# Optimization experiments

Hardware: AMD Instinct MI355X
Metric: run time of the kernel (lower is better)

Reference implementation:

```python
import jax, jax.numpy as jnp
import numpy as np

B, S, D, H = 2, 2048, 512, 8
HD = D // H  # head_size = 64
EPS = 1e-5


def _layer_norm(x, g, b):
    m = jnp.mean(x, axis=-1, keepdims=True)
    v = jnp.mean(jnp.square(x - m), axis=-1, keepdims=True)
    return (x - m) * jax.lax.rsqrt(v + EPS) * g + b


def setup_inputs() -> dict:
    key = jax.random.key(0)
    ks = jax.random.split(key, 16)
    s_in = 1.0 / np.sqrt(D)
    s_ff = 1.0 / np.sqrt(4 * D)
    return {
        "x": jax.random.normal(ks[0], (B, S, D), jnp.float32),
        # per-head q/k/v projections stacked over heads: [H, D, HD]
        "Wq": jax.random.normal(ks[1], (H, D, HD), jnp.float32) * s_in,
        "bq": jax.random.normal(ks[2], (H, HD), jnp.float32) * s_in,
        "Wk": jax.random.normal(ks[3], (H, D, HD), jnp.float32) * s_in,
        "bk": jax.random.normal(ks[4], (H, HD), jnp.float32) * s_in,
        "Wv": jax.random.normal(ks[5], (H, D, HD), jnp.float32) * s_in,
        "bv": jax.random.normal(ks[6], (H, HD), jnp.float32) * s_in,
        "Wp": jax.random.normal(ks[7], (D, D), jnp.float32) * s_in,
        "bp": jax.random.normal(ks[8], (D,), jnp.float32) * s_in,
        "W1": jax.random.normal(ks[9], (D, 4 * D), jnp.float32) * s_in,
        "b1": jax.random.normal(ks[10], (4 * D,), jnp.float32) * s_in,
        "W2": jax.random.normal(ks[11], (4 * D, D), jnp.float32) * s_ff,
        "b2": jax.random.normal(ks[12], (D,), jnp.float32) * s_ff,
        "g1": jnp.ones((D,), jnp.float32),
        "be1": jnp.zeros((D,), jnp.float32),
        "g2": jnp.ones((D,), jnp.float32),
        "be2": jnp.zeros((D,), jnp.float32),
    }


def reference(x, Wq, bq, Wk, bk, Wv, bv, Wp, bp, W1, b1, W2, b2, g1, be1, g2, be2):
    # --- attention sublayer (pre-norm) ---
    xn = _layer_norm(x, g1, be1)                               # [B,S,D]
    q = jnp.einsum('bsd,hde->bhse', xn, Wq) + bq[None, :, None, :]
    k = jnp.einsum('bsd,hde->bhse', xn, Wk) + bk[None, :, None, :]
    v = jnp.einsum('bsd,hde->bhse', xn, Wv) + bv[None, :, None, :]
    # NOTE: original has NO 1/sqrt(head_size) scaling and NO mask
    scores = jnp.einsum('bhse,bhte->bhst', q, k)               # [B,H,S,S]
    w = jax.nn.softmax(scores, axis=-1)
    o = jnp.einsum('bhst,bhte->bhse', w, v)                    # [B,H,S,HD]
    o = o.transpose(0, 2, 1, 3).reshape(x.shape[0], x.shape[1], D)  # concat heads
    attn_out = o @ Wp + bp
    x = x + attn_out
    # --- MLP sublayer (pre-norm) ---
    xn2 = _layer_norm(x, g2, be2)
    h = jax.nn.relu(xn2 @ W1 + b1)
    x = x + (h @ W2 + b2)
    return x
```

## Files before the change

### kernel.cpp

```cpp
#include <hip/hip_runtime.h>
#include <hip/hip_bf16.h>

typedef unsigned short u16;
typedef unsigned long long u64t;
typedef __attribute__((ext_vector_type(8))) short bhalf8;
typedef __attribute__((ext_vector_type(4))) short bhalf4;
typedef __attribute__((ext_vector_type(4))) float f32x4;

#define MFMA16(a, b, c) __builtin_amdgcn_mfma_f32_16x16x32_bf16((a), (b), (c), 0, 0, 0)

#if __has_builtin(__builtin_amdgcn_mfma_f32_16x16x16bf16_1k)
#define HAVE_K16 1
#define MFMAK16(a, b, c) __builtin_amdgcn_mfma_f32_16x16x16bf16_1k((a), (b), (c), 0, 0, 0)
#elif __has_builtin(__builtin_amdgcn_mfma_f32_16x16x16_bf16)
#define HAVE_K16 1
#define MFMAK16(a, b, c) __builtin_amdgcn_mfma_f32_16x16x16_bf16((a), (b), (c), 0, 0, 0)
#else
#define HAVE_K16 0
#endif

#define BB 2
#define SS 2048
#define DD 512
#define HH 8
#define HD 64
#define NT (BB * SS)
#define LOG2E 1.44269504f

#if __has_builtin(__builtin_amdgcn_exp2f)
#define EXP2(x) __builtin_amdgcn_exp2f(x)
#else
#define EXP2(x) exp2f(x)
#endif

__device__ __forceinline__ u16 f2b(float f) {
    unsigned u = __builtin_bit_cast(unsigned, f);
    unsigned r = (u + 0x7fffu + ((u >> 16) & 1u)) >> 16;
    return (u16)r;
}

__device__ __forceinline__ void gl2lds16(const u16* g, u16* l) {
    u16* gn = (u16*)g;
    __builtin_amdgcn_global_load_lds((__attribute__((address_space(1))) void*)gn,
                                     (__attribute__((address_space(3))) void*)l, 16, 0, 0);
}

__global__ __launch_bounds__(256) void k_prep(const float* __restrict__ Wq, const float* __restrict__ Wk,
                                              const float* __restrict__ Wv, const float* __restrict__ Wp,
                                              const float* __restrict__ W1, const float* __restrict__ W2,
                                              const float* __restrict__ bq, const float* __restrict__ bk,
                                              const float* __restrict__ bv,
                                              u16* __restrict__ WqkvT, u16* __restrict__ WpT,
                                              u16* __restrict__ W1T, u16* __restrict__ W2T,
                                              float* __restrict__ biasqkv,
                                              const float* __restrict__ x, const float* __restrict__ g1,
                                              const float* __restrict__ be1, u16* __restrict__ xn) {
    int j = blockIdx.x;
    int t = threadIdx.x;
    if (j >= 3078) {
        int wave = t >> 6, lane = t & 63;
        int row = (j - 3078) * 4 + wave;
        const float* xr = x + (size_t)row * DD;
        int c = lane * 8;
        float4 v0 = *(const float4*)(xr + c);
        float4 v1 = *(const float4*)(xr + c + 4);
        float s  = v0.x + v0.y + v0.z + v0.w + v1.x + v1.y + v1.z + v1.w;
        float sq = v0.x*v0.x + v0.y*v0.y + v0.z*v0.z + v0.w*v0.w
                 + v1.x*v1.x + v1.y*v1.y + v1.z*v1.z + v1.w*v1.w;
#pragma unroll
        for (int m = 1; m < 64; m <<= 1) {
            s  += __shfl_xor(s, m);
            sq += __shfl_xor(sq, m);
        }
        float mean = s * (1.0f / DD);
        float var  = sq * (1.0f / DD) - mean * mean;
        float rstd = rsqrtf(var + 1e-5f);
        float4 g0 = *(const float4*)(g1 + c);
        float4 g4 = *(const float4*)(g1 + c + 4);
        float4 b0 = *(const float4*)(be1 + c);
        float4 b4 = *(const float4*)(be1 + c + 4);
        float xv[8] = {v0.x, v0.y, v0.z, v0.w, v1.x, v1.y, v1.z, v1.w};
        float gv[8] = {g0.x, g0.y, g0.z, g0.w, g4.x, g4.y, g4.z, g4.w};
        float bv2[8] = {b0.x, b0.y, b0.z, b0.w, b4.x, b4.y, b4.z, b4.w};
        union { bhalf8 v; u16 u[8]; } pk;
#pragma unroll
        for (int i = 0; i < 8; i++) pk.u[i] = f2b((xv[i] - mean) * rstd * gv[i] + bv2[i]);
        *(bhalf8*)(xn + (size_t)row * DD + c) = pk.v;
        return;
    }
    int tx = t & 31, ty = t >> 5;
    if (j >= 3072) {
        int i = (j - 3072) * 256 + ty * 32 + tx;
        biasqkv[i] = (i < 512) ? bq[i] : (i < 1024) ? bk[i - 512] : bv[i - 1024];
        return;
    }
    __shared__ float tile[32][33];
    const float* src; u16* dst; int R, C, tr, tc;
    if (j < 768) {
        int m = j >> 8, rem = j & 255, h = rem >> 5, tl = rem & 31;
        tr = tl >> 1; tc = tl & 1;
        src = (m == 0 ? Wq : (m == 1 ? Wk : Wv)) + h * 32768;
        dst = WqkvT + m * 262144 + h * 32768;
        R = 512; C = 64;
    } else if (j < 1024) { int tl = j - 768;  tr = tl >> 4; tc = tl & 15; src = Wp; dst = WpT; R = 512;  C = 512;  }
    else if (j < 2048)   { int tl = j - 1024; tr = tl >> 6; tc = tl & 63; src = W1; dst = W1T; R = 512;  C = 2048; }
    else                 { int tl = j - 2048; tr = tl >> 4; tc = tl & 15; src = W2; dst = W2T; R = 2048; C = 512;  }
    int c = tc * 32 + tx;
#pragma unroll
    for (int i = 0; i < 4; i++)
        tile[ty + i * 8][tx] = src[(size_t)(tr * 32 + ty + i * 8) * C + c];
    __syncthreads();
    int r2 = tr * 32 + tx;
#pragma unroll
    for (int i = 0; i < 4; i++)
        dst[(size_t)(tc * 32 + ty + i * 8) * R + r2] = f2b(tile[tx][ty + i * 8]);
}

__global__ __launch_bounds__(256) void k_layernorm(const float* __restrict__ x,
                                                   const float* __restrict__ g,
                                                   const float* __restrict__ be,
                                                   u16* __restrict__ out) {
    int wave = threadIdx.x >> 6, lane = threadIdx.x & 63;
    int row = blockIdx.x * 4 + wave;
    const float* xr = x + (size_t)row * DD;
    int c = lane * 8;
    float4 v0 = *(const float4*)(xr + c);
    float4 v1 = *(const float4*)(xr + c + 4);
    float s  = v0.x + v0.y + v0.z + v0.w + v1.x + v1.y + v1.z + v1.w;
    float sq = v0.x*v0.x + v0.y*v0.y + v0.z*v0.z + v0.w*v0.w
             + v1.x*v1.x + v1.y*v1.y + v1.z*v1.z + v1.w*v1.w;
#pragma unroll
    for (int m = 1; m < 64; m <<= 1) {
        s  += __shfl_xor(s, m);
        sq += __shfl_xor(sq, m);
    }
    float mean = s * (1.0f / DD);
    float var  = sq * (1.0f / DD) - mean * mean;
    float rstd = rsqrtf(var + 1e-5f);
    float4 g0 = *(const float4*)(g + c);
    float4 g1 = *(const float4*)(g + c + 4);
    float4 b0 = *(const float4*)(be + c);
    float4 b1 = *(const float4*)(be + c + 4);
    float xv[8] = {v0.x, v0.y, v0.z, v0.w, v1.x, v1.y, v1.z, v1.w};
    float gv[8] = {g0.x, g0.y, g0.z, g0.w, g1.x, g1.y, g1.z, g1.w};
    float bv[8] = {b0.x, b0.y, b0.z, b0.w, b1.x, b1.y, b1.z, b1.w};
    union { bhalf8 v; u16 u[8]; } pk;
#pragma unroll
    for (int i = 0; i < 8; i++) pk.u[i] = f2b((xv[i] - mean) * rstd * gv[i] + bv[i]);
    *(bhalf8*)(out + (size_t)row * DD + c) = pk.v;
}

template<int BM, int BN, int WR, int WC, int MI, int NI, int MODE>
__global__ __launch_bounds__(256) void k_gemm(const u16* __restrict__ A, const u16* __restrict__ Bt,
                                              const float* __restrict__ bias,
                                              int lda, int ldb, int kLen, int N,
                                              const float* __restrict__ resid,
                                              float* __restrict__ outF, u16* __restrict__ outB,
                                              u16* __restrict__ qd, u16* __restrict__ kd,
                                              u16* __restrict__ vtd) {
    constexpr int WM = MI * 16;
    constexpr int WN = NI * 16;
    static_assert(WR * WM == BM && WC * WN == BN && WR * WC == 4, "cfg");
    constexpr int ACH = BM / 32;
    constexpr int BCH = BN / 32;
    __shared__ u16 As[BM * 64];
    __shared__ u16 Bs[BN * 64];
    int t = threadIdx.x;
    int wave = t >> 6, lane = t & 63, quad = lane >> 4, l16 = lane & 15;
    int wr, wc;
    if (WC == 1)      { wr = wave; wc = 0; }
    else if (WR == 1) { wr = 0;    wc = wave; }
    else              { wr = wave >> 1; wc = wave & 1; }
    int m0 = blockIdx.y * BM, n0 = blockIdx.x * BN;

    f32x4 acc[MI][NI] = {};

    int srow = lane >> 3;
    int scol = (lane & 7) * 8;
    const u16* Ag = A  + (size_t)(m0 + srow) * lda + scol;
    const u16* Bg = Bt + (size_t)(n0 + srow) * ldb + scol;

    for (int k0 = 0; k0 < kLen; k0 += 64) {
        __syncthreads();
#pragma unroll
        for (int c = 0; c < ACH; c++) {
            int ch = wave * ACH + c;
            gl2lds16(Ag + (size_t)(ch * 8) * lda + k0, &As[ch * 512]);
        }
#pragma unroll
        for (int c = 0; c < BCH; c++) {
            int ch = wave * BCH + c;
            gl2lds16(Bg + (size_t)(ch * 8) * ldb + k0, &Bs[ch * 512]);
        }
        __syncthreads();
#pragma unroll
        for (int h = 0; h < 2; h++) {
            bhalf8 af[MI], bf[NI];
#pragma unroll
            for (int mi = 0; mi < MI; mi++)
                af[mi] = *(bhalf8*)&As[(wr * WM + mi * 16 + l16) * 64 + h * 32 + quad * 8];
#pragma unroll
            for (int ni = 0; ni < NI; ni++)
                bf[ni] = *(bhalf8*)&Bs[(wc * WN + ni * 16 + l16) * 64 + h * 32 + quad * 8];
#pragma unroll
            for (int mi = 0; mi < MI; mi++)
#pragma unroll
                for (int ni = 0; ni < NI; ni++)
                    acc[mi][ni] = MFMA16(af[mi], bf[ni], acc[mi][ni]);
        }
    }

#pragma unroll
    for (int mi = 0; mi < MI; mi++)
#pragma unroll
        for (int ni = 0; ni < NI; ni++) {
            f32x4 a = acc[mi][ni];
            int gc = n0 + wc * WN + ni * 16 + l16;
            int gr0 = m0 + wr * WM + mi * 16 + quad * 4;
            float bsv = bias[gc];
            if (MODE == 0) {
                int mm = gc >> 9, cc = gc & 511;
                int hh = cc >> 6, e = cc & 63;
                int b = gr0 >> 11, s0 = gr0 & 2047;
                if (mm == 2) {
                    u64t pk = 0;
#pragma unroll
                    for (int r = 0; r < 4; r++) pk |= (u64t)f2b(a[r] + bsv) << (16 * r);
                    *(u64t*)&vtd[((size_t)(b * HH + hh) * HD + e) * SS + s0] = pk;
                } else if (mm == 0) {
#pragma unroll
                    for (int r = 0; r < 4; r++)
                        qd[((size_t)(b * HH + hh) * SS + s0 + r) * HD + e] = f2b((a[r] + bsv) * LOG2E);
                } else {
#pragma unroll
                    for (int r = 0; r < 4; r++)
                        kd[((size_t)(b * HH + hh) * SS + s0 + r) * HD + e] = f2b(a[r] + bsv);
                }
            } else if (MODE == 1) {
#pragma unroll
                for (int r = 0; r < 4; r++) {
                    size_t idx = (size_t)(gr0 + r) * N + gc;
                    outF[idx] = a[r] + bsv + resid[idx];
                }
            } else {
#pragma unroll
                for (int r = 0; r < 4; r++)
                    outB[(size_t)(gr0 + r) * N + gc] = f2b(fmaxf(a[r] + bsv, 0.0f));
            }
        }
}

__global__ __launch_bounds__(512) void k_attention(const u16* __restrict__ q,
                                                   const u16* __restrict__ k,
                                                   const u16* __restrict__ vt,
                                                   float* __restrict__ Opart,
                                                   float* __restrict__ lsum) {
    __shared__ u16 sm[17920];
    u16* Ks = sm;
    u16* Vs = sm + 9216;
    float* Ored = (float*)sm;
    float* Lred = (float*)sm + 8192;

    int bh = blockIdx.x, qt = blockIdx.y, kspl = blockIdx.z;
    int t = threadIdx.x, wave = t >> 6, lane = t & 63, quad = lane >> 4, l16 = lane & 15;
    int g = wave >> 2, qw = wave & 3;
    const u16* qb = q  + (size_t)bh * SS * HD;
    const u16* kb = k  + (size_t)bh * SS * HD;
    const u16* vb = vt + (size_t)bh * HD * SS;

    bhalf8 qfa0, qfa1, qfb0, qfb1;
    {
        int r0 = qt * 128 + qw * 32 + l16;
        qfa0 = *(const bhalf8*)(qb + (size_t)r0 * HD + quad * 8);
        qfa1 = *(const bhalf8*)(qb + (size_t)r0 * HD + 32 + quad * 8);
        qfb0 = *(const bhalf8*)(qb + (size_t)(r0 + 16) * HD + quad * 8);
        qfb1 = *(const bhalf8*)(qb + (size_t)(r0 + 16) * HD + 32 + quad * 8);
    }

    f32x4 oacc[2][4] = {};
    float rsa = 0.f, rsb = 0.f;

    int kr = t >> 2, kc = (t & 3) * 16;
    int vr = t >> 3, vc = (t & 7) * 16;
    const u16* kp = kb + ((size_t)kspl * 1024 + kr) * HD + kc;
    const u16* vp = vb + (size_t)vr * SS + kspl * 1024 + vc;
    u16* ksd = &Ks[kr * 72 + kc];
    u16* vsd = &Vs[vr * 136 + vc];

    bhalf8 kreg[2], vreg[2];
#pragma unroll
    for (int i = 0; i < 2; i++) {
        kreg[i] = *(const bhalf8*)(kp + i * 8);
        vreg[i] = *(const bhalf8*)(vp + i * 8);
    }

    for (int it = 0; it < 8; it++) {
        __syncthreads();
#pragma unroll
        for (int i = 0; i < 2; i++) {
            *(bhalf8*)(ksd + i * 8) = kreg[i];
            *(bhalf8*)(vsd + i * 8) = vreg[i];
        }
        __syncthreads();
        if (it < 7) {
            const u16* kn = kp + (size_t)(it + 1) * 128 * HD;
            const u16* vn = vp + (it + 1) * 128;
#pragma unroll
            for (int i = 0; i < 2; i++) {
                kreg[i] = *(const bhalf8*)(kn + i * 8);
                vreg[i] = *(const bhalf8*)(vn + i * 8);
            }
        }

#pragma unroll
        for (int nt2 = 0; nt2 < 4; nt2++) {
            int nt = g * 4 + nt2;
            bhalf8 kf0 = *(bhalf8*)&Ks[(nt * 16 + l16) * 72 + quad * 8];
            bhalf8 kf1 = *(bhalf8*)&Ks[(nt * 16 + l16) * 72 + 32 + quad * 8];
            f32x4 sa = {}, sb = {};
            sa = MFMA16(kf0, qfa0, sa);
            sa = MFMA16(kf1, qfa1, sa);
            sb = MFMA16(kf0, qfb0, sb);
            sb = MFMA16(kf1, qfb1, sb);
#if HAVE_K16
            union { bhalf4 v; u16 u[4]; } pa, pb;
#pragma unroll
            for (int r = 0; r < 4; r++) {
                float p0 = EXP2(sa[r]);
                float p1 = EXP2(sb[r]);
                rsa += p0; rsb += p1;
                pa.u[r] = f2b(p0); pb.u[r] = f2b(p1);
            }
#pragma unroll
            for (int et = 0; et < 4; et++) {
                bhalf4 vf = *(bhalf4*)&Vs[(et * 16 + l16) * 136 + nt * 16 + quad * 4];
                oacc[0][et] = MFMAK16(pa.v, vf, oacc[0][et]);
                oacc[1][et] = MFMAK16(pb.v, vf, oacc[1][et]);
            }
#else
            union { bhalf8 v; u16 u[8]; } pa, pb;
#pragma unroll
            for (int r = 0; r < 4; r++) {
                float p0 = EXP2(sa[r]);
                float p1 = EXP2(sb[r]);
                rsa += p0; rsb += p1;
                pa.u[r] = f2b(p0); pb.u[r] = f2b(p1);
            }
#pragma unroll
            for (int r = 4; r < 8; r++) { pa.u[r] = 0; pb.u[r] = 0; }
#pragma unroll
            for (int et = 0; et < 4; et++) {
                union { bhalf8 v; bhalf4 h[2]; } vf;
                vf.h[0] = *(bhalf4*)&Vs[(et * 16 + l16) * 136 + nt * 16 + quad * 4];
                vf.h[1] = (bhalf4){0, 0, 0, 0};
                oacc[0][et] = MFMA16(pa.v, vf.v, oacc[0][et]);
                oacc[1][et] = MFMA16(pb.v, vf.v, oacc[1][et]);
            }
#endif
        }
    }

    rsa += __shfl_xor(rsa, 16); rsa += __shfl_xor(rsa, 32);
    rsb += __shfl_xor(rsb, 16); rsb += __shfl_xor(rsb, 32);

    __syncthreads();
    if (g == 1) {
#pragma unroll
        for (int qc = 0; qc < 2; qc++)
#pragma unroll
            for (int et = 0; et < 4; et++)
#pragma unroll
                for (int r = 0; r < 4; r++)
                    Ored[(qw * 32 + qc * 16 + quad * 4 + r) * 64 + et * 16 + l16] = oacc[qc][et][r];
        if (quad == 0) {
            Lred[qw * 32 + l16]      = rsa;
            Lred[qw * 32 + 16 + l16] = rsb;
        }
    }
    __syncthreads();
    if (g == 0) {
#pragma unroll
        for (int qc = 0; qc < 2; qc++) {
            int sbase = qt * 128 + qw * 32 + qc * 16;
            float* Ob = Opart + ((size_t)(kspl * 16 + bh) * SS + sbase) * HD;
#pragma unroll
            for (int et = 0; et < 4; et++)
#pragma unroll
                for (int r = 0; r < 4; r++) {
                    float v = oacc[qc][et][r]
                            + Ored[(qw * 32 + qc * 16 + quad * 4 + r) * 64 + et * 16 + l16];
                    Ob[(quad * 4 + r) * HD + et * 16 + l16] = v;
                }
            if (quad == 0)
                lsum[(size_t)(kspl * 16 + bh) * SS + sbase + l16] =
                    (qc == 0 ? rsa : rsb) + Lred[qw * 32 + qc * 16 + l16];
        }
    }
}

__global__ __launch_bounds__(256) void k_combine(const float* __restrict__ Opart,
                                                 const float* __restrict__ lsum,
                                                 u16* __restrict__ oc) {
    int tid = blockIdx.x * 256 + threadIdx.x;
    int c4 = tid & 15, s = (tid >> 4) & 2047, bh = tid >> 15;
    size_t i0 = ((size_t)bh * SS + s) * HD + c4 * 4;
    float4 p0 = *(const float4*)(Opart + i0);
    float4 p1 = *(const float4*)(Opart + (size_t)16 * SS * HD + i0);
    float l = lsum[(size_t)bh * SS + s] + lsum[(size_t)16 * SS + (size_t)bh * SS + s];
    float inv = 1.0f / l;
    u64t pk = 0;
    pk |= (u64t)f2b((p0.x + p1.x) * inv);
    pk |= (u64t)f2b((p0.y + p1.y) * inv) << 16;
    pk |= (u64t)f2b((p0.z + p1.z) * inv) << 32;
    pk |= (u64t)f2b((p0.w + p1.w) * inv) << 48;
    int b = bh >> 3, h = bh & 7;
    *(u64t*)&oc[((size_t)b * SS + s) * DD + h * HD + c4 * 4] = pk;
}

extern "C" void kernel_launch(void* const* d_in, const int* in_sizes, int n_in,
                              void* d_out, int out_size, void* d_ws, size_t ws_size,
                              hipStream_t stream) {
    const float* x   = (const float*)d_in[0];
    const float* Wq  = (const float*)d_in[1];
    const float* bq  = (const float*)d_in[2];
    const float* Wk  = (const float*)d_in[3];
    const float* bk  = (const float*)d_in[4];
    const float* Wv  = (const float*)d_in[5];
    const float* bv  = (const float*)d_in[6];
    const float* Wp  = (const float*)d_in[7];
    const float* bp  = (const float*)d_in[8];
    const float* W1  = (const float*)d_in[9];
    const float* b1  = (const float*)d_in[10];
    const float* W2  = (const float*)d_in[11];
    const float* b2  = (const float*)d_in[12];
    const float* g1  = (const float*)d_in[13];
    const float* be1 = (const float*)d_in[14];
    const float* g2  = (const float*)d_in[15];
    const float* be2 = (const float*)d_in[16];

    char* ws = (char*)d_ws;
    u16*   WqkvT   = (u16*)(ws + 0);
    u16*   WpT     = (u16*)(ws + 1572864);
    u16*   W1T     = (u16*)(ws + 2097152);
    u16*   W2T     = (u16*)(ws + 4194304);
    float* biasqkv = (float*)(ws + 6291456);
    u16*   xn      = (u16*)(ws + 6297600);
    u16*   qB      = (u16*)(ws + 10491904);
    u16*   kB      = (u16*)(ws + 14686208);
    u16*   vTb     = (u16*)(ws + 18880512);
    u16*   oc      = (u16*)(ws + 23074816);
    float* x1      = (float*)(ws + 27269120);
    u16*   xn2     = (u16*)(ws + 35657728);
    u16*   hbuf    = (u16*)(ws + 39852032);
    float* Opart   = (float*)hbuf;
    float* lsum    = (float*)xn;

    k_prep<<<4102, 256, 0, stream>>>(Wq, Wk, Wv, Wp, W1, W2, bq, bk, bv,
                                     WqkvT, WpT, W1T, W2T, biasqkv,
                                     x, g1, be1, xn);
    k_gemm<128, 128, 2, 2, 4, 4, 0><<<dim3(12, 32), 256, 0, stream>>>(
        xn, WqkvT, biasqkv, 512, 512, 512, 1536, nullptr, nullptr, nullptr, qB, kB, vTb);
    k_attention<<<dim3(16, 16, 2), 512, 0, stream>>>(qB, kB, vTb, Opart, lsum);
    k_combine<<<2048, 256, 0, stream>>>(Opart, lsum, oc);
    k_gemm<64, 64, 2, 2, 2, 2, 1><<<dim3(8, 64), 256, 0, stream>>>(
        oc, WpT, bp, 512, 512, 512, 512, x, x1, nullptr, nullptr, nullptr, nullptr);
    k_layernorm<<<NT / 4, 256, 0, stream>>>(x1, g2, be2, xn2);
    k_gemm<128, 128, 2, 2, 4, 4, 2><<<dim3(16, 32), 256, 0, stream>>>(
        xn2, W1T, b1, 512, 512, 512, 2048, nullptr, nullptr, hbuf, nullptr, nullptr, nullptr);
    k_gemm<64, 64, 2, 2, 2, 2, 1><<<dim3(8, 64), 256, 0, stream>>>(
        hbuf, W2T, b2, 2048, 2048, 2048, 512, x1, (float*)d_out, nullptr, nullptr, nullptr, nullptr);
}
```

Measured before the change: 209.1 us.

## Split-K the W2 GEMM with atomics and pre-initialize output in layernorm

The final MLP down-projection GEMM (K=2048) now uses a 128x64 tile with split-K over two z-slices, accumulating partial results into the output with atomicAdd. The second layernorm kernel writes residual plus b2 into the output buffer beforehand, so the GEMM adds no bias or residual. The attention kernel also keeps per-register row-sum accumulators instead of a single scalar, which shortens the dependency chain. The trade-off is float atomic traffic and a nondeterministic summation order in exchange for different tiling and more parallelism in the K dimension.

```diff
diff --git a/kernel.cpp b/kernel.cpp
--- a/kernel.cpp
+++ b/kernel.cpp
@@ -119,13 +119,23 @@
 __global__ __launch_bounds__(256) void k_layernorm(const float* __restrict__ x,
                                                    const float* __restrict__ g,
                                                    const float* __restrict__ be,
-                                                   u16* __restrict__ out) {
+                                                   u16* __restrict__ out,
+                                                   const float* __restrict__ b2,
+                                                   float* __restrict__ outInit) {
     int wave = threadIdx.x >> 6, lane = threadIdx.x & 63;
     int row = blockIdx.x * 4 + wave;
     const float* xr = x + (size_t)row * DD;
     int c = lane * 8;
     float4 v0 = *(const float4*)(xr + c);
     float4 v1 = *(const float4*)(xr + c + 4);
+    {
+        float4 ba = *(const float4*)(b2 + c);
+        float4 bb = *(const float4*)(b2 + c + 4);
+        float4 o0 = {v0.x + ba.x, v0.y + ba.y, v0.z + ba.z, v0.w + ba.w};
+        float4 o1 = {v1.x + bb.x, v1.y + bb.y, v1.z + bb.z, v1.w + bb.w};
+        *(float4*)(outInit + (size_t)row * DD + c) = o0;
+        *(float4*)(outInit + (size_t)row * DD + c + 4) = o1;
+    }
     float s  = v0.x + v0.y + v0.z + v0.w + v1.x + v1.y + v1.z + v1.w;
     float sq = v0.x*v0.x + v0.y*v0.y + v0.z*v0.z + v0.w*v0.w
              + v1.x*v1.x + v1.y*v1.y + v1.z*v1.z + v1.w*v1.w;
@@ -172,13 +182,14 @@
     else if (WR == 1) { wr = 0;    wc = wave; }
     else              { wr = wave >> 1; wc = wave & 1; }
     int m0 = blockIdx.y * BM, n0 = blockIdx.x * BN;
+    int kOff = blockIdx.z * kLen;
 
     f32x4 acc[MI][NI] = {};
 
     int srow = lane >> 3;
     int scol = (lane & 7) * 8;
-    const u16* Ag = A  + (size_t)(m0 + srow) * lda + scol;
-    const u16* Bg = Bt + (size_t)(n0 + srow) * ldb + scol;
+    const u16* Ag = A  + (size_t)(m0 + srow) * lda + scol + kOff;
+    const u16* Bg = Bt + (size_t)(n0 + srow) * ldb + scol + kOff;
 
     for (int k0 = 0; k0 < kLen; k0 += 64) {
         __syncthreads();
@@ -217,7 +228,7 @@
             f32x4 a = acc[mi][ni];
             int gc = n0 + wc * WN + ni * 16 + l16;
             int gr0 = m0 + wr * WM + mi * 16 + quad * 4;
-            float bsv = bias[gc];
+            float bsv = (MODE == 3) ? 0.0f : bias[gc];
             if (MODE == 0) {
                 int mm = gc >> 9, cc = gc & 511;
                 int hh = cc >> 6, e = cc & 63;
@@ -242,10 +253,14 @@
                     size_t idx = (size_t)(gr0 + r) * N + gc;
                     outF[idx] = a[r] + bsv + resid[idx];
                 }
-            } else {
+            } else if (MODE == 2) {
 #pragma unroll
                 for (int r = 0; r < 4; r++)
                     outB[(size_t)(gr0 + r) * N + gc] = f2b(fmaxf(a[r] + bsv, 0.0f));
+            } else {
+#pragma unroll
+                for (int r = 0; r < 4; r++)
+                    atomicAdd(&outF[(size_t)(gr0 + r) * N + gc], a[r]);
             }
         }
 }
@@ -278,7 +293,7 @@
     }
 
     f32x4 oacc[2][4] = {};
-    float rsa = 0.f, rsb = 0.f;
+    f32x4 rsa4 = {}, rsb4 = {};
 
     int kr = t >> 2, kc = (t & 3) * 16;
     int vr = t >> 3, vc = (t & 7) * 16;
@@ -328,7 +343,7 @@
             for (int r = 0; r < 4; r++) {
                 float p0 = EXP2(sa[r]);
                 float p1 = EXP2(sb[r]);
-                rsa += p0; rsb += p1;
+                rsa4[r] += p0; rsb4[r] += p1;
                 pa.u[r] = f2b(p0); pb.u[r] = f2b(p1);
             }
 #pragma unroll
@@ -343,7 +358,7 @@
             for (int r = 0; r < 4; r++) {
                 float p0 = EXP2(sa[r]);
                 float p1 = EXP2(sb[r]);
-                rsa += p0; rsb += p1;
+                rsa4[r] += p0; rsb4[r] += p1;
                 pa.u[r] = f2b(p0); pb.u[r] = f2b(p1);
             }
 #pragma unroll
@@ -360,6 +375,8 @@
         }
     }
 
+    float rsa = (rsa4[0] + rsa4[1]) + (rsa4[2] + rsa4[3]);
+    float rsb = (rsb4[0] + rsb4[1]) + (rsb4[2] + rsb4[3]);
     rsa += __shfl_xor(rsa, 16); rsa += __shfl_xor(rsa, 32);
     rsb += __shfl_xor(rsb, 16); rsb += __shfl_xor(rsb, 32);
 
@@ -464,9 +481,9 @@
     k_combine<<<2048, 256, 0, stream>>>(Opart, lsum, oc);
     k_gemm<64, 64, 2, 2, 2, 2, 1><<<dim3(8, 64), 256, 0, stream>>>(
         oc, WpT, bp, 512, 512, 512, 512, x, x1, nullptr, nullptr, nullptr, nullptr);
-    k_layernorm<<<NT / 4, 256, 0, stream>>>(x1, g2, be2, xn2);
+    k_layernorm<<<NT / 4, 256, 0, stream>>>(x1, g2, be2, xn2, b2, (float*)d_out);
     k_gemm<128, 128, 2, 2, 4, 4, 2><<<dim3(16, 32), 256, 0, stream>>>(
         xn2, W1T, b1, 512, 512, 512, 2048, nullptr, nullptr, hbuf, nullptr, nullptr, nullptr);
-    k_gemm<64, 64, 2, 2, 2, 2, 1><<<dim3(8, 64), 256, 0, stream>>>(
-        hbuf, W2T, b2, 2048, 2048, 2048, 512, x1, (float*)d_out, nullptr, nullptr, nullptr, nullptr);
-}
+    k_gemm<128, 64, 2, 2, 4, 2, 3><<<dim3(8, 32, 2), 256, 0, stream>>>(
+        hbuf, W2T, b2, 2048, 2048, 1024, 512, nullptr, (float*)d_out, nullptr, nullptr, nullptr, nullptr);
+}
```

Result: slower. 215.5 us (+3.1%).
